# Optimization experiments

Measured on AMD Instinct MI355X. Metric: run time of the kernel, lower is better.

The kernel has to match this reference:

```python
import jax, jax.numpy as jnp
import numpy as np
from jax import lax

N_COMPONENTS = 50
K = 15
SIGMA = 1.0
N_ITERS = 100


def _pairwise_sq_dists(x):
    # squared euclidean distances, [N, N]
    sq = jnp.sum(x * x, axis=1)
    d2 = sq[:, None] + sq[None, :] - 2.0 * (x @ x.T)
    return jnp.maximum(d2, 0.0)


def _knn_affinity(d2, scale):
    # top-K smallest distances per row -> dense sparse-pattern affinity, row-normalized
    n = d2.shape[0]
    neg_topk, knn_idx = lax.top_k(-d2, K)          # [N, K]
    w = jnp.exp(-(-neg_topk) * scale)              # exp(-d^2 * scale) on kNN entries
    rows = jnp.arange(n)[:, None]
    mat = jnp.zeros_like(d2).at[rows, knn_idx].set(w)
    return mat / jnp.sum(mat, axis=1, keepdims=True)


def setup_inputs() -> dict:
    key = jax.random.key(0)
    expression = jax.random.normal(key, (4096, 1000), dtype=jnp.float32)
    return {"expression": expression}


def reference(expression):
    x = expression
    n = x.shape[0]

    # --- PCA via eigh of gene-gene covariance ---
    xc = x - jnp.mean(x, axis=0)
    cov = (xc.T @ xc) / (n - 1)                    # [G, G]
    evals, evecs = jnp.linalg.eigh(cov)            # ascending
    order = jnp.argsort(evals)[::-1]
    evecs = evecs[:, order]
    pca = xc @ evecs[:, :N_COMPONENTS]             # [N, C]

    d2 = _pairwise_sq_dists(pca)                   # [N, N]

    # transition matrix: exp(-d^2 / (2 sigma^2)) on kNN
    transition = _knn_affinity(d2, 1.0 / (2.0 * SIGMA ** 2))
    # pseudotime diffusion matrix: exp(-d^2) on kNN
    diff_mat = _knn_affinity(d2, 1.0)

    # power iteration from root cell 0
    d0 = jnp.zeros((n,), dtype=pca.dtype).at[0].set(1.0)

    def step(d, _):
        dn = diff_mat @ d
        dn = dn / jnp.max(dn)
        return dn, None

    pseudotime, _ = lax.scan(step, d0, None, length=N_ITERS)

    return (pseudotime.astype(jnp.float32),
            transition.astype(jnp.float32),
            pca.astype(jnp.float32))
```

## Files before the change

### kernel.cpp

```cpp
#include <hip/hip_runtime.h>
#include <math.h>
#include <stdint.h>

static const int NS = 4096;
static const int MF = 1000;
static const int NCOMP = 50;

#define TR_OFF  ((size_t)4096)
#define PCA_OFF ((size_t)4096 + (size_t)4096*4096)

__global__ void k_colsum(const float* __restrict__ x, float* __restrict__ part){
  int b = blockIdx.x, tid = threadIdx.x;
  float a0=0,a1=0,a2=0,a3=0;
  for (int r=b*64; r<b*64+64; r++){
    const float* row = x + (size_t)r*MF;
    if (tid      < MF) a0 += row[tid];
    if (tid+256  < MF) a1 += row[tid+256];
    if (tid+512  < MF) a2 += row[tid+512];
    if (tid+768  < MF) a3 += row[tid+768];
  }
  if (tid      < MF) part[b*MF+tid]     = a0;
  if (tid+256  < MF) part[b*MF+tid+256] = a1;
  if (tid+512  < MF) part[b*MF+tid+512] = a2;
  if (tid+768  < MF) part[b*MF+tid+768] = a3;
}

__global__ void k_colmean(const float* __restrict__ part, float* __restrict__ mean){
  int c = blockIdx.x*256 + threadIdx.x;
  if (c < MF){ float s=0; for (int b=0;b<64;b++) s += part[b*MF+c]; mean[c] = s/4096.0f; }
}

__global__ void k_cov(const float* __restrict__ x, const float* __restrict__ mean,
                      double* __restrict__ Ah){
  __shared__ float As[32][65];
  __shared__ float Bs[32][65];
  int i0 = blockIdx.y*64, j0 = blockIdx.x*64;
  int tx = threadIdx.x, ty = threadIdx.y;
  int tid = ty*16+tx;
  double acc[4][4];
  #pragma unroll
  for (int u=0;u<4;u++)
    #pragma unroll
    for (int v=0;v<4;v++) acc[u][v]=0.0;
  for (int k0=0;k0<4096;k0+=32){
    for (int t=tid;t<32*64;t+=256){
      int kk=t>>6, ii=t&63;
      int gi=i0+ii, gj=j0+ii;
      As[kk][ii] = (gi<MF) ? (x[(size_t)(k0+kk)*MF+gi]-mean[gi]) : 0.f;
      Bs[kk][ii] = (gj<MF) ? (x[(size_t)(k0+kk)*MF+gj]-mean[gj]) : 0.f;
    }
    __syncthreads();
    for (int kk=0;kk<32;kk++){
      float a[4], b[4];
      #pragma unroll
      for (int u=0;u<4;u++){ a[u]=As[kk][ty*4+u]; b[u]=Bs[kk][tx*4+u]; }
      #pragma unroll
      for (int u=0;u<4;u++)
        #pragma unroll
        for (int v=0;v<4;v++) acc[u][v] += (double)a[u]*(double)b[v];
    }
    __syncthreads();
  }
  #pragma unroll
  for (int u=0;u<4;u++)
    #pragma unroll
    for (int v=0;v<4;v++){
      int gi=i0+ty*4+u, gj=j0+tx*4+v;
      if (gi<MF && gj<MF) Ah[(size_t)gi*MF+gj] = acc[u][v]*(1.0/4095.0);
    }
}

__device__ __forceinline__ unsigned wang(unsigned s){
  s=(s^61u)^(s>>16); s*=9u; s^=s>>4; s*=0x27d4eb2du; s^=s>>15; return s;
}

__global__ void __launch_bounds__(256) k_hh_step(double* __restrict__ Ah,
                                                 double* __restrict__ Vh,
                                                 double* __restrict__ tauv,
                                                 double* __restrict__ betaH,
                                                 const double* __restrict__ w1prev,
                                                 double* __restrict__ w1next,
                                                 const double* __restrict__ colprev,
                                                 double* __restrict__ colnext,
                                                 int k){
  __shared__ double vprev[1000], wfull[1000], vk[1000];
  __shared__ double red4[4], redb[4];
  int tid = threadIdx.x;
  int lane = tid & 63, wv = tid >> 6;

  double vd = 0.0;
  if (k > 0){
    for (int j = k + tid; j < 1000; j += 256){
      double vv = Vh[(size_t)(k-1)*MF + j];
      double ww = w1prev[j];
      vprev[j] = vv;
      wfull[j] = ww;
      vd += vv*ww;
    }
  }
  #pragma unroll
  for (int off=32; off; off>>=1) vd += __shfl_down(vd, off, 64);
  if (lane==0) red4[wv] = vd;
  __syncthreads();
  double vdot = red4[0]+red4[1]+red4[2]+red4[3];
  double tp  = (k>0) ? tauv[k-1] : 0.0;
  double hts = 0.5*tp*tp*vdot;
  if (k > 0){
    for (int j = k + tid; j < 1000; j += 256)
      wfull[j] = tp*wfull[j] - hts*vprev[j];
  }
  __syncthreads();

  double a2 = 0.0;
  for (int j = k+1 + tid; j < 1000; j += 256){
    double c;
    if (k > 0) c = colprev[j] - (vprev[j]*wfull[k] + wfull[j]*vprev[k]);
    else       c = Ah[(size_t)j*MF + k];
    vk[j] = c;
    if (j > k+1) a2 += c*c;
  }
  #pragma unroll
  for (int off=32; off; off>>=1) a2 += __shfl_down(a2, off, 64);
  if (lane==0) redb[wv] = a2;
  __syncthreads();
  double xn2 = redb[0]+redb[1]+redb[2]+redb[3];
  double alpha = vk[k+1];
  double beta, tau, scl;
  if (xn2 == 0.0){ beta = alpha; tau = 0.0; scl = 0.0; }
  else {
    double nrm = sqrt(alpha*alpha + xn2);
    beta = (alpha >= 0.0) ? -nrm : nrm;
    tau  = (beta - alpha)/beta;
    scl  = 1.0/(alpha - beta);
  }
  if (tid==0 && blockIdx.x==0){
    tauv[k]=tau; betaH[k]=beta;
    if (k>0) Ah[(size_t)k*MF + k] -= 2.0*wfull[k];
  }
  for (int j = k+1 + tid; j < 1000; j += 256)
    vk[j] = (j == k+1) ? 1.0 : vk[j]*scl;
  __syncthreads();
  if (blockIdx.x==0){
    for (int j = k+1 + tid; j < 1000; j += 256)
      Vh[(size_t)k*MF + j] = vk[j];
  }

  int step = gridDim.x*4;
  for (int r = k+1 + blockIdx.x*4 + wv; r < 1000; r += step){
    double vr = (k>0)? vprev[r] : 0.0;
    double wr = (k>0)? wfull[r] : 0.0;
    double* row = Ah + (size_t)r*MF;
    double acc = 0.0;
    for (int c = k+1 + lane; c < 1000; c += 64){
      double a = row[c];
      if (k > 0){
        a -= vr*wfull[c] + wr*vprev[c];
        row[c] = a;
      }
      acc += a*vk[c];
      if (c == k+1) colnext[r] = a;
    }
    #pragma unroll
    for (int off=32; off; off>>=1) acc += __shfl_down(acc, off, 64);
    if (lane==0) w1next[r] = acc;
  }
}

__global__ void k_hh_fin(double* __restrict__ Ah, const double* __restrict__ Vh,
                         const double* __restrict__ tauv,
                         const double* __restrict__ w1last){
  if (threadIdx.x==0 && blockIdx.x==0){
    double v8 = Vh[(size_t)997*MF + 998];
    double v9 = Vh[(size_t)997*MF + 999];
    double w18 = w1last[998], w19 = w1last[999];
    double tau = tauv[997];
    double vdot = v8*w18 + v9*w19;
    double hts = 0.5*tau*tau*vdot;
    double w8 = tau*w18 - hts*v8;
    double w9 = tau*w19 - hts*v9;
    Ah[(size_t)998*MF+998] -= v8*w8 + w8*v8;
    Ah[(size_t)999*MF+998] -= v9*w8 + w9*v8;
    Ah[(size_t)999*MF+999] -= v9*w9 + w9*v9;
  }
}

__global__ void k_hh_extract(const double* __restrict__ Ah, double* __restrict__ alphaH,
                             double* __restrict__ betaH){
  int t = blockIdx.x*256 + threadIdx.x;
  if (t < MF) alphaH[t] = Ah[(size_t)t*MF+t];
  if (t == 0) betaH[998] = Ah[(size_t)999*MF+998];
}

__device__ __forceinline__ int sgnchg(double a, double b){
  return (int)(((unsigned long long)(__double_as_longlong(a) ^ __double_as_longlong(b))) >> 63);
}

__global__ void k_bisect(const double* __restrict__ alphaT, const double* __restrict__ betaT,
                         double* __restrict__ lamT){
  __shared__ double al[1000], ab[1000], bb[1000];
  int tid = threadIdx.x;
  for (int t=tid; t<1000; t+=64){
    double a = alphaT[t];
    double b = (t<999)? betaT[t] : 0.0;
    al[t]=a; ab[t]=fabs(b); bb[t]=b*b;
  }
  __syncthreads();
  if (tid >= NCOMP) return;
  int i = tid;
  double lo=1e300, hi=-1e300;
  for (int k2=0;k2<1000;k2++){
    double bl = (k2>0)? ab[k2-1] : 0.0;
    double br = (k2<999)? ab[k2] : 0.0;
    double a = al[k2];
    lo = fmin(lo, a-bl-br);
    hi = fmax(hi, a+bl+br);
  }
  int target = 999 - i;
  for (int it=0; it<55; it++){
    double mid = 0.5*(lo+hi);
    int cnt = 0;
    double d1 = 1.0;
    double d0 = al[0]-mid;
    cnt += (int)(((unsigned long long)__double_as_longlong(d0))>>63);
    int k2 = 1;
    for (; k2+3 < 1000; k2 += 4){
      double n0 = (al[k2  ]-mid)*d0 - bb[k2-1]*d1;
      double n1 = (al[k2+1]-mid)*n0 - bb[k2  ]*d0;
      double n2 = (al[k2+2]-mid)*n1 - bb[k2+1]*n0;
      double n3 = (al[k2+3]-mid)*n2 - bb[k2+2]*n1;
      cnt += sgnchg(n0,d0)+sgnchg(n1,n0)+sgnchg(n2,n1)+sgnchg(n3,n2);
      double mm = fmax(fabs(n3), fabs(n2));
      double s = (mm > 1e250) ? 1e-250 : ((mm < 1e-250) ? 1e250 : 1.0);
      d1 = n2*s; d0 = n3*s;
    }
    for (; k2 < 1000; k2++){
      double nn = (al[k2]-mid)*d0 - bb[k2-1]*d1;
      cnt += sgnchg(nn, d0);
      d1 = d0; d0 = nn;
    }
    if (cnt > target) hi = mid; else lo = mid;
  }
  lamT[i] = 0.5*(lo+hi);
}

__device__ void gtsv_serial(int m, double* dl, double* dd, double* du, double* x){
  for (int r=0;r<m-1;r++){
    if (fabs(dd[r]) >= fabs(dl[r])){
      if (dd[r] != 0.0){
        double fact = dl[r]/dd[r];
        dd[r+1] -= fact*du[r];
        x[r+1]  -= fact*x[r];
      }
      if (r < m-2) dl[r] = 0.0;
    } else {
      double fact = dd[r]/dl[r];
      dd[r] = dl[r];
      double tdd = dd[r+1];
      dd[r+1] = du[r] - fact*tdd;
      if (r < m-2){
        double tdu = du[r+1];
        dl[r] = tdu;
        du[r+1] = -fact*tdu;
      }
      du[r] = tdd;
      double t2 = x[r]; x[r] = x[r+1]; x[r+1] = t2 - fact*x[r+1];
    }
  }
  x[m-1] /= dd[m-1];
  if (m >= 2) x[m-2] = (x[m-2] - du[m-2]*x[m-1])/dd[m-2];
  for (int r=m-3;r>=0;r--)
    x[r] = (x[r] - du[r]*x[r+1] - dl[r]*x[r+2])/dd[r];
}

__global__ void __launch_bounds__(256) k_inviter(const double* __restrict__ alphaH,
                                                 const double* __restrict__ betaH,
                                                 const double* __restrict__ lamT,
                                                 double* __restrict__ V50,
                                                 double* __restrict__ lamR){
  __shared__ double v[1000], xx[1000], dd[1000], du[1000], dl[1000];
  __shared__ double red[256];
  int i = blockIdx.x, tid = threadIdx.x;
  double lam = lamT[i];
  for (int t=tid;t<1000;t+=256){
    unsigned h = wang((unsigned)(i*1000+t)*2654435761u + 777u);
    v[t] = (double)(h & 0xffffffu)/8388608.0 - 1.0;
  }
  __syncthreads();
  for (int it=0; it<3; it++){
    for (int t=tid;t<1000;t+=256){
      dd[t] = alphaH[t]-lam;
      if (t<999){ du[t]=betaH[t]; dl[t]=betaH[t]; }
      xx[t] = v[t];
    }
    __syncthreads();
    if (tid==0) gtsv_serial(1000, dl, dd, du, xx);
    __syncthreads();
    double a=0; for (int t=tid;t<1000;t+=256) a += xx[t]*xx[t];
    red[tid]=a; __syncthreads();
    for (int off=128;off;off>>=1){ if(tid<off) red[tid]+=red[tid+off]; __syncthreads(); }
    double inv = 1.0/sqrt(red[0]);
    __syncthreads();
    for (int t=tid;t<1000;t+=256) v[t]=xx[t]*inv;
    __syncthreads();
  }
  double a=0;
  for (int t=tid;t<1000;t+=256){
    double s = alphaH[t]*v[t];
    if (t>0)   s += betaH[t-1]*v[t-1];
    if (t<999) s += betaH[t]*v[t+1];
    a += v[t]*s;
  }
  red[tid]=a; __syncthreads();
  for (int off=128;off;off>>=1){ if(tid<off) red[tid]+=red[tid+off]; __syncthreads(); }
  if (tid==0) lamR[i]=red[0];
  for (int t=tid;t<1000;t+=256) V50[(size_t)i*1000+t]=v[t];
}

__global__ void __launch_bounds__(256) k_sign(const double* __restrict__ alphaH,
                                              const double* __restrict__ betaH,
                                              const double* __restrict__ V50,
                                              const double* __restrict__ lamR,
                                              float* __restrict__ sgnv){
  __shared__ double v[1000], xx[1000], dd[1000], du[1000], dl[1000];
  __shared__ double red[256];
  __shared__ double lam_s;
  __shared__ int ab[2];
  __shared__ float sig;
  int i = blockIdx.x, tid = threadIdx.x;
  for (int t=tid;t<1000;t+=256) v[t]=V50[(size_t)i*1000+t];
  if (tid==0){ lam_s=lamR[i]; ab[0]=0; ab[1]=1000; sig=1.f; }
  __syncthreads();
  while (true){
    int a=ab[0], b=ab[1];
    if (b-a <= 25) break;
    int c = a + (b-a)/2;
    double m1=0,m2=0;
    for (int t=a+tid;t<b;t+=256){ double q=v[t]*v[t]; if (t<c) m1+=q; else m2+=q; }
    red[tid]=m1; __syncthreads();
    for (int off=128;off;off>>=1){ if(tid<off) red[tid]+=red[tid+off]; __syncthreads(); }
    double M1=red[0]; __syncthreads();
    red[tid]=m2; __syncthreads();
    for (int off=128;off;off>>=1){ if(tid<off) red[tid]+=red[tid+off]; __syncthreads(); }
    double M2=red[0]; __syncthreads();
    double tot=M1+M2;
    if (fmin(M1,M2) <= 1e-10*tot){
      if (tid==0){ if (M1>=M2) ab[1]=c; else ab[0]=c; }
      __syncthreads();
      a=ab[0]; b=ab[1];
      double nn=0; for (int t=a+tid;t<b;t+=256) nn+=v[t]*v[t];
      red[tid]=nn; __syncthreads();
      for (int off=128;off;off>>=1){ if(tid<off) red[tid]+=red[tid+off]; __syncthreads(); }
      double inv = 1.0/sqrt(red[0]); __syncthreads();
      for (int t=a+tid;t<b;t+=256) v[t]*=inv;
      __syncthreads();
      for (int it=0; it<2; it++){
        for (int t=a+tid;t<b;t+=256){
          int L=t-a;
          dd[L]=alphaH[t]-lam_s;
          if (t<b-1){ du[L]=betaH[t]; dl[L]=betaH[t]; }
          xx[L]=v[t];
        }
        __syncthreads();
        if (tid==0) gtsv_serial(b-a, dl, dd, du, xx);
        __syncthreads();
        double s2=0; for (int t=a+tid;t<b;t+=256){ double q=xx[t-a]; s2+=q*q; }
        red[tid]=s2; __syncthreads();
        for (int off=128;off;off>>=1){ if(tid<off) red[tid]+=red[tid+off]; __syncthreads(); }
        double inv2 = 1.0/sqrt(red[0]); __syncthreads();
        for (int t=a+tid;t<b;t+=256) v[t]=xx[t-a]*inv2;
        __syncthreads();
      }
      double rq=0;
      for (int t=a+tid;t<b;t+=256){
        double s = alphaH[t]*v[t];
        if (t>a)   s += betaH[t-1]*v[t-1];
        if (t<b-1) s += betaH[t]*v[t+1];
        rq += v[t]*s;
      }
      red[tid]=rq; __syncthreads();
      for (int off=128;off;off>>=1){ if(tid<off) red[tid]+=red[tid+off]; __syncthreads(); }
      if (tid==0) lam_s=red[0];
      __syncthreads();
      continue;
    }
    if (tid==0){
      double vc1 = v[c-1], vc = v[c];
      if (fabs(vc1) >= fabs(vc)){
        sig = (vc1 < 0.0) ? 1.f : -1.f;
      } else {
        double req = (betaH[c-1] >= 0.0) ? -1.0 : 1.0;
        double have = (vc >= 0.0) ? 1.0 : -1.0;
        sig = (have == req) ? 1.f : -1.f;
      }
    }
    break;
  }
  __syncthreads();
  if (tid==0) sgnv[i]=sig;
}

__global__ void __launch_bounds__(256) k_applyQm(const double* __restrict__ Vh,
                                                 const double* __restrict__ tauv,
                                                 const double* __restrict__ V50,
                                                 const float* __restrict__ sgnv,
                                                 float* __restrict__ E50){
  __shared__ double u[1000];
  __shared__ double red4[4];
  int i = blockIdx.x, tid = threadIdx.x;
  int lane = tid & 63, wv = tid >> 6;
  for (int t=tid;t<1000;t+=256) u[t] = V50[(size_t)i*1000+t];
  __syncthreads();
  for (int k=997;k>=0;k--){
    const double* v = Vh + (size_t)k*MF;
    double vr[4];
    double a=0;
    #pragma unroll
    for (int s=0;s<4;s++){
      int j = k+1+tid+s*256;
      double vv = 0.0;
      if (j < 1000){ vv = v[j]; a += vv*u[j]; }
      vr[s] = vv;
    }
    #pragma unroll
    for (int off=32; off; off>>=1) a += __shfl_down(a, off, 64);
    if (lane==0) red4[wv] = a;
    __syncthreads();
    double td = tauv[k]*(red4[0]+red4[1]+red4[2]+red4[3]);
    #pragma unroll
    for (int s=0;s<4;s++){
      int j = k+1+tid+s*256;
      if (j < 1000) u[j] -= td*vr[s];
    }
    __syncthreads();
  }
  double s = (double)sgnv[i];
  for (int t=tid;t<1000;t+=256) E50[(size_t)t*NCOMP + i] = (float)(u[t]*s);
}

__global__ void k_pca(const float* __restrict__ x, const float* __restrict__ mean,
                      const float* __restrict__ E, float* __restrict__ P){
  __shared__ float As[64][65];
  __shared__ float Es[64][65];
  int r0 = blockIdx.x*64;
  int tx = threadIdx.x & 15, ty = threadIdx.x >> 4;
  float acc[4][4];
  #pragma unroll
  for (int u=0;u<4;u++)
    #pragma unroll
    for (int v=0;v<4;v++) acc[u][v]=0.f;
  for (int k0=0;k0<MF;k0+=64){
    for (int t=threadIdx.x;t<64*64;t+=256){
      int i=t>>6, kk=t&63; int k=k0+kk;
      As[i][kk] = (k<MF) ? (x[(size_t)(r0+i)*MF+k]-mean[k]) : 0.f;
    }
    for (int t=threadIdx.x;t<64*65;t+=256){
      int kk=t/65, c=t%65; int k=k0+kk;
      Es[kk][c] = (k<MF && c<NCOMP) ? E[(size_t)k*NCOMP+c] : 0.f;
    }
    __syncthreads();
    for (int kk=0;kk<64;kk++){
      float a[4], b[4];
      #pragma unroll
      for (int u=0;u<4;u++){ a[u]=As[ty*4+u][kk]; b[u]=Es[kk][tx*4+u]; }
      #pragma unroll
      for (int u=0;u<4;u++)
        #pragma unroll
        for (int v=0;v<4;v++) acc[u][v] += a[u]*b[v];
    }
    __syncthreads();
  }
  #pragma unroll
  for (int u=0;u<4;u++){
    int r=r0+ty*4+u;
    #pragma unroll
    for (int v=0;v<4;v++){
      int c=tx*4+v;
      if (c<NCOMP) P[(size_t)r*NCOMP+c] = acc[u][v];
    }
  }
}

__global__ void k_rowsq(const float* __restrict__ P, float* __restrict__ sqv){
  int r = blockIdx.x*256 + threadIdx.x;
  if (r < NS){
    float s=0;
    for (int c=0;c<NCOMP;c++){ float v=P[(size_t)r*NCOMP+c]; s+=v*v; }
    sqv[r]=s;
  }
}

__global__ void k_knn(const float* __restrict__ P, const float* __restrict__ sqv,
                      float* __restrict__ trans, int* __restrict__ kidx,
                      float* __restrict__ kwd){
  __shared__ float pi[64];
  __shared__ unsigned long long keys[16*256];
  __shared__ unsigned long long redk[4];
  __shared__ unsigned long long wink[15];
  __shared__ float wt[15], wd[15], sums[2];
  int i = blockIdx.x, tid = threadIdx.x;
  int lane = tid & 63, wv = tid >> 6;
  for (int t=tid;t<NCOMP;t+=256) pi[t] = P[(size_t)i*NCOMP+t];
  __syncthreads();
  float sqi = sqv[i];
  for (int s2=0;s2<16;s2++){
    int j = tid + s2*256;
    float dot=0;
    for (int c=0;c<NCOMP;c++) dot += pi[c]*P[(size_t)j*NCOMP+c];
    float d2 = sqi + sqv[j] - 2.f*dot;
    d2 = fmaxf(d2, 0.f);
    unsigned int db = __float_as_uint(d2);
    keys[s2*256+tid] = ((unsigned long long)db<<32) | (unsigned)j;
  }
  __syncthreads();
  for (int rsel=0;rsel<15;rsel++){
    unsigned long long m = ~0ull;
    #pragma unroll
    for (int s2=0;s2<16;s2++){
      unsigned long long k = keys[s2*256+tid];
      m = (k<m)?k:m;
    }
    #pragma unroll
    for (int off=32; off; off>>=1){
      unsigned long long o = __shfl_down(m, off, 64);
      m = (o<m)?o:m;
    }
    if (lane==0) redk[wv]=m;
    __syncthreads();
    unsigned long long w = redk[0];
    if (redk[1]<w) w=redk[1];
    if (redk[2]<w) w=redk[2];
    if (redk[3]<w) w=redk[3];
    if (tid==0) wink[rsel]=w;
    #pragma unroll
    for (int s2=0;s2<16;s2++)
      if (keys[s2*256+tid]==w) keys[s2*256+tid]=~0ull;
    __syncthreads();
  }
  if (tid<15){
    unsigned long long w = wink[tid];
    float d2 = __uint_as_float((unsigned)(w>>32));
    wt[tid] = expf(-0.5f*d2);
    wd[tid] = expf(-d2);
  }
  __syncthreads();
  if (tid==0){
    float st=0, sd=0;
    for (int k=0;k<15;k++){ st+=wt[k]; sd+=wd[k]; }
    sums[0]=st; sums[1]=sd;
  }
  __syncthreads();
  float* row = trans + (size_t)i*NS;
  for (int c=tid;c<NS;c+=256) row[c]=0.f;
  __syncthreads();
  if (tid<15){
    int j = (int)(wink[tid] & 0xffffffffull);
    row[j] = wt[tid]/sums[0];
    kidx[i*15+tid] = j;
    kwd[i*15+tid]  = wd[tid]/sums[1];
  }
}

__global__ void __launch_bounds__(1024) k_power(const int* __restrict__ kidx,
                                                const float* __restrict__ kwd,
                                                float* __restrict__ outPT){
  __shared__ float d[4096];
  __shared__ float dn[4096];
  __shared__ float red[16];
  int tid = threadIdx.x;
  int lane = tid & 63, wv = tid >> 6;
  for (int t=tid;t<4096;t+=1024) d[t] = (t==0)?1.f:0.f;
  __syncthreads();
  for (int it=0; it<100; it++){
    float lmax = 0.f;
    for (int r=tid;r<4096;r+=1024){
      float a=0;
      #pragma unroll
      for (int k=0;k<15;k++) a += kwd[r*15+k]*d[kidx[r*15+k]];
      dn[r]=a;
      lmax = fmaxf(lmax, a);
    }
    #pragma unroll
    for (int off=32; off; off>>=1) lmax = fmaxf(lmax, __shfl_down(lmax, off, 64));
    if (lane==0) red[wv]=lmax;
    __syncthreads();
    float m = red[0];
    #pragma unroll
    for (int w=1;w<16;w++) m = fmaxf(m, red[w]);
    for (int r=tid;r<4096;r+=1024) d[r]=dn[r]/m;
    __syncthreads();
  }
  for (int t=tid;t<4096;t+=1024) outPT[t]=d[t];
}

extern "C" void kernel_launch(void* const* d_in, const int* in_sizes, int n_in,
                              void* d_out, int out_size, void* d_ws, size_t ws_size,
                              hipStream_t stream){
  const float* x = (const float*)d_in[0];
  float* out = (float*)d_out;
  char* base = (char*)d_ws;

  double* Ah     = (double*)(base + 0);
  float*  sqv    = (float*) (base + 0);
  int*    kidx   = (int*)   (base + 16384);
  float*  kwd    = (float*) (base + 262144);
  double* Vh     = (double*)(base + 8000000);
  double* V50    = (double*)(base + 16000000);
  float*  E50    = (float*) (base + 16400000);
  float*  part   = (float*) (base + 16600000);
  float*  mean   = (float*) (base + 16856000);
  double* tauv   = (double*)(base + 16860000);
  double* betaH  = (double*)(base + 16868000);
  double* alphaH = (double*)(base + 16876000);
  double* w1a    = (double*)(base + 16884000);
  double* w1b    = (double*)(base + 16892000);
  double* cola   = (double*)(base + 16900000);
  double* colb   = (double*)(base + 16908000);
  double* lamT   = (double*)(base + 16916000);
  double* lamR   = (double*)(base + 16916400);
  float*  sgnv   = (float*) (base + 16916800);

  double* w1buf[2]  = { w1a, w1b };
  double* colbuf[2] = { cola, colb };

  k_colsum<<<64,256,0,stream>>>(x, part);
  k_colmean<<<4,256,0,stream>>>(part, mean);
  k_cov<<<dim3(16,16),dim3(16,16),0,stream>>>(x, mean, Ah);

  for (int k=0;k<998;k++){
    int m = 999-k;
    int g = (m+3)>>2;
    if (g > 250) g = 250;
    k_hh_step<<<g,256,0,stream>>>(Ah, Vh, tauv, betaH,
        w1buf[(k+1)&1], w1buf[k&1], colbuf[(k+1)&1], colbuf[k&1], k);
  }
  k_hh_fin<<<1,64,0,stream>>>(Ah, Vh, tauv, w1buf[997&1]);
  k_hh_extract<<<4,256,0,stream>>>(Ah, alphaH, betaH);

  k_bisect<<<1,64,0,stream>>>(alphaH, betaH, lamT);
  k_inviter<<<50,256,0,stream>>>(alphaH, betaH, lamT, V50, lamR);

  k_sign<<<50,256,0,stream>>>(alphaH, betaH, V50, lamR, sgnv);

  k_applyQm<<<50,256,0,stream>>>(Vh, tauv, V50, sgnv, E50);
  k_pca<<<64,256,0,stream>>>(x, mean, E50, out + PCA_OFF);
  k_rowsq<<<16,256,0,stream>>>(out + PCA_OFF, sqv);
  k_knn<<<4096,256,0,stream>>>(out + PCA_OFF, sqv, out + TR_OFF, kidx, kwd);
  k_power<<<1,1024,0,stream>>>(kidx, kwd, out);
}
```

Baseline: 15.82 ms.

## Fuse Householder tridiagonalization into one persistent kernel with grid barrier

Replaces 998 separate Householder step launches with one persistent 250-block kernel that synchronizes through an atomic grid barrier, keeping the previous reflector in shared memory. It also computes only the lower-triangular covariance tiles and mirrors them. It merges the finalize, extract and bisection kernels, and merges inverse iteration with sign fixing. applyQm now keeps the vector in registers with one barrier per step. The aim is to remove per-launch overhead and redundant work. The risk is that the software grid barrier deadlocks if all 250 blocks are not co-resident, and the spinning and fences add cost at every step.

New measurement: 39.51 ms. 150% more time.

```diff
diff --git a/kernel.cpp b/kernel.cpp
--- a/kernel.cpp
+++ b/kernel.cpp
@@ -8,6 +8,7 @@
 
 #define TR_OFF  ((size_t)4096)
 #define PCA_OFF ((size_t)4096 + (size_t)4096*4096)
+#define HH_GRID 250
 
 __global__ void k_colsum(const float* __restrict__ x, float* __restrict__ part){
   int b = blockIdx.x, tid = threadIdx.x;
@@ -30,11 +31,15 @@
   if (c < MF){ float s=0; for (int b=0;b<64;b++) s += part[b*MF+c]; mean[c] = s/4096.0f; }
 }
 
+__global__ void k_barinit(unsigned* bar){ if (threadIdx.x < 2) bar[threadIdx.x] = 0u; }
+
 __global__ void k_cov(const float* __restrict__ x, const float* __restrict__ mean,
                       double* __restrict__ Ah){
   __shared__ float As[32][65];
   __shared__ float Bs[32][65];
-  int i0 = blockIdx.y*64, j0 = blockIdx.x*64;
+  int bx = blockIdx.x, by = blockIdx.y;
+  if (bx > by) return;
+  int i0 = by*64, j0 = bx*64;
   int tx = threadIdx.x, ty = threadIdx.y;
   int tid = ty*16+tx;
   double acc[4][4];
@@ -66,7 +71,11 @@
     #pragma unroll
     for (int v=0;v<4;v++){
       int gi=i0+ty*4+u, gj=j0+tx*4+v;
-      if (gi<MF && gj<MF) Ah[(size_t)gi*MF+gj] = acc[u][v]*(1.0/4095.0);
+      if (gi<MF && gj<MF){
+        double val = acc[u][v]*(1.0/4095.0);
+        Ah[(size_t)gi*MF+gj] = val;
+        Ah[(size_t)gj*MF+gi] = val;
+      }
     }
 }
 
@@ -74,102 +83,135 @@
   s=(s^61u)^(s>>16); s*=9u; s^=s>>4; s*=0x27d4eb2du; s^=s>>15; return s;
 }
 
-__global__ void __launch_bounds__(256) k_hh_step(double* __restrict__ Ah,
-                                                 double* __restrict__ Vh,
-                                                 double* __restrict__ tauv,
-                                                 double* __restrict__ betaH,
-                                                 const double* __restrict__ w1prev,
-                                                 double* __restrict__ w1next,
-                                                 const double* __restrict__ colprev,
-                                                 double* __restrict__ colnext,
-                                                 int k){
-  __shared__ double vprev[1000], wfull[1000], vk[1000];
+__device__ __forceinline__ void grid_sync(unsigned* bar){
+  __syncthreads();
+  if (threadIdx.x == 0){
+    __threadfence();
+    unsigned gen = __hip_atomic_load(&bar[1], __ATOMIC_RELAXED, __HIP_MEMORY_SCOPE_AGENT);
+    unsigned prev = __hip_atomic_fetch_add(&bar[0], 1u, __ATOMIC_ACQ_REL, __HIP_MEMORY_SCOPE_AGENT);
+    if (prev + 1u == (unsigned)HH_GRID){
+      __hip_atomic_store(&bar[0], 0u, __ATOMIC_RELAXED, __HIP_MEMORY_SCOPE_AGENT);
+      __hip_atomic_fetch_add(&bar[1], 1u, __ATOMIC_RELEASE, __HIP_MEMORY_SCOPE_AGENT);
+    } else {
+      while (__hip_atomic_load(&bar[1], __ATOMIC_RELAXED, __HIP_MEMORY_SCOPE_AGENT) == gen)
+        __builtin_amdgcn_s_sleep(1);
+    }
+    __threadfence();
+  }
+  __syncthreads();
+}
+
+__global__ void __launch_bounds__(256) k_hh_all(double* Ah,
+                                                double* __restrict__ Vh,
+                                                double* __restrict__ tauv,
+                                                double* __restrict__ betaH,
+                                                double* w1a, double* w1b,
+                                                double* cola, double* colb,
+                                                unsigned* bar){
+  __shared__ double vbuf[2][1000];
+  __shared__ double wfull[1000];
   __shared__ double red4[4], redb[4];
+  __shared__ double sAlpha;
   int tid = threadIdx.x;
   int lane = tid & 63, wv = tid >> 6;
-
-  double vd = 0.0;
-  if (k > 0){
-    for (int j = k + tid; j < 1000; j += 256){
-      double vv = Vh[(size_t)(k-1)*MF + j];
-      double ww = w1prev[j];
-      vprev[j] = vv;
-      wfull[j] = ww;
-      vd += vv*ww;
-    }
-  }
-  #pragma unroll
-  for (int off=32; off; off>>=1) vd += __shfl_down(vd, off, 64);
-  if (lane==0) red4[wv] = vd;
-  __syncthreads();
-  double vdot = red4[0]+red4[1]+red4[2]+red4[3];
-  double tp  = (k>0) ? tauv[k-1] : 0.0;
-  double hts = 0.5*tp*tp*vdot;
-  if (k > 0){
-    for (int j = k + tid; j < 1000; j += 256)
-      wfull[j] = tp*wfull[j] - hts*vprev[j];
-  }
-  __syncthreads();
-
-  double a2 = 0.0;
-  for (int j = k+1 + tid; j < 1000; j += 256){
-    double c;
-    if (k > 0) c = colprev[j] - (vprev[j]*wfull[k] + wfull[j]*vprev[k]);
-    else       c = Ah[(size_t)j*MF + k];
-    vk[j] = c;
-    if (j > k+1) a2 += c*c;
-  }
-  #pragma unroll
-  for (int off=32; off; off>>=1) a2 += __shfl_down(a2, off, 64);
-  if (lane==0) redb[wv] = a2;
-  __syncthreads();
-  double xn2 = redb[0]+redb[1]+redb[2]+redb[3];
-  double alpha = vk[k+1];
-  double beta, tau, scl;
-  if (xn2 == 0.0){ beta = alpha; tau = 0.0; scl = 0.0; }
-  else {
-    double nrm = sqrt(alpha*alpha + xn2);
-    beta = (alpha >= 0.0) ? -nrm : nrm;
-    tau  = (beta - alpha)/beta;
-    scl  = 1.0/(alpha - beta);
-  }
-  if (tid==0 && blockIdx.x==0){
-    tauv[k]=tau; betaH[k]=beta;
-    if (k>0) Ah[(size_t)k*MF + k] -= 2.0*wfull[k];
-  }
-  for (int j = k+1 + tid; j < 1000; j += 256)
-    vk[j] = (j == k+1) ? 1.0 : vk[j]*scl;
-  __syncthreads();
-  if (blockIdx.x==0){
+  double tau_prev = 0.0;
+
+  for (int k = 0; k < 998; k++){
+    double* vk    = vbuf[k & 1];
+    double* vprev = vbuf[(k & 1) ^ 1];
+    const double* w1prev  = (k & 1) ? w1a : w1b;
+    double*       w1next  = (k & 1) ? w1b : w1a;
+    const double* colprev = (k & 1) ? cola : colb;
+    double*       colnext = (k & 1) ? colb : cola;
+
+    double vd = 0.0;
+    if (k > 0){
+      for (int j = k + tid; j < 1000; j += 256){
+        double ww = w1prev[j];
+        wfull[j] = ww;
+        vd += vprev[j]*ww;
+      }
+    }
+    #pragma unroll
+    for (int off=32; off; off>>=1) vd += __shfl_down(vd, off, 64);
+    if (lane==0) red4[wv] = vd;
+    __syncthreads();
+    double vdot = red4[0]+red4[1]+red4[2]+red4[3];
+    double tp  = tau_prev;
+    double hts = 0.5*tp*tp*vdot;
+    if (k > 0){
+      for (int j = k + tid; j < 1000; j += 256)
+        wfull[j] = tp*wfull[j] - hts*vprev[j];
+    }
+    __syncthreads();
+
+    double a2 = 0.0;
+    for (int j = k+1 + tid; j < 1000; j += 256){
+      double c;
+      if (k > 0) c = colprev[j] - (vprev[j]*wfull[k] + wfull[j]*vprev[k]);
+      else       c = Ah[(size_t)j*MF + k];
+      vk[j] = c;
+      if (j == k+1) sAlpha = c;
+      if (j > k+1) a2 += c*c;
+    }
+    #pragma unroll
+    for (int off=32; off; off>>=1) a2 += __shfl_down(a2, off, 64);
+    if (lane==0) redb[wv] = a2;
+    __syncthreads();
+    double xn2 = redb[0]+redb[1]+redb[2]+redb[3];
+    double alpha = sAlpha;
+    double beta, tau, scl;
+    if (xn2 == 0.0){ beta = alpha; tau = 0.0; scl = 0.0; }
+    else {
+      double nrm = sqrt(alpha*alpha + xn2);
+      beta = (alpha >= 0.0) ? -nrm : nrm;
+      tau  = (beta - alpha)/beta;
+      scl  = 1.0/(alpha - beta);
+    }
+    if (tid==0 && blockIdx.x==0){
+      tauv[k]=tau; betaH[k]=beta;
+      if (k>0) Ah[(size_t)k*MF + k] -= 2.0*wfull[k];
+    }
     for (int j = k+1 + tid; j < 1000; j += 256)
-      Vh[(size_t)k*MF + j] = vk[j];
-  }
-
-  int step = gridDim.x*4;
-  for (int r = k+1 + blockIdx.x*4 + wv; r < 1000; r += step){
-    double vr = (k>0)? vprev[r] : 0.0;
-    double wr = (k>0)? wfull[r] : 0.0;
-    double* row = Ah + (size_t)r*MF;
-    double acc = 0.0;
-    for (int c = k+1 + lane; c < 1000; c += 64){
-      double a = row[c];
-      if (k > 0){
-        a -= vr*wfull[c] + wr*vprev[c];
-        row[c] = a;
-      }
-      acc += a*vk[c];
-      if (c == k+1) colnext[r] = a;
-    }
-    #pragma unroll
-    for (int off=32; off; off>>=1) acc += __shfl_down(acc, off, 64);
-    if (lane==0) w1next[r] = acc;
-  }
-}
-
-__global__ void k_hh_fin(double* __restrict__ Ah, const double* __restrict__ Vh,
-                         const double* __restrict__ tauv,
-                         const double* __restrict__ w1last){
-  if (threadIdx.x==0 && blockIdx.x==0){
+      vk[j] = (j == k+1) ? 1.0 : vk[j]*scl;
+    __syncthreads();
+    if (blockIdx.x==0){
+      for (int j = k+1 + tid; j < 1000; j += 256)
+        Vh[(size_t)k*MF + j] = vk[j];
+    }
+
+    for (int r = k+1 + blockIdx.x*4 + wv; r < 1000; r += HH_GRID*4){
+      double vr = (k>0)? vprev[r] : 0.0;
+      double wr = (k>0)? wfull[r] : 0.0;
+      double* row = Ah + (size_t)r*MF;
+      double acc = 0.0;
+      for (int c = k+1 + lane; c < 1000; c += 64){
+        double a = row[c];
+        if (k > 0){ a -= vr*wfull[c] + wr*vprev[c]; row[c] = a; }
+        acc += a*vk[c];
+        if (c == k+1) colnext[r] = a;
+      }
+      #pragma unroll
+      for (int off=32; off; off>>=1) acc += __shfl_down(acc, off, 64);
+      if (lane==0) w1next[r] = acc;
+    }
+
+    grid_sync(bar);
+    tau_prev = tau;
+  }
+}
+
+__device__ __forceinline__ int sgnchg(double a, double b){
+  return (int)(((unsigned long long)(__double_as_longlong(a) ^ __double_as_longlong(b))) >> 63);
+}
+
+__global__ void k_post(double* __restrict__ Ah, const double* __restrict__ Vh,
+                       const double* __restrict__ tauv, const double* __restrict__ w1last,
+                       double* __restrict__ alphaH, double* __restrict__ betaH,
+                       double* __restrict__ lamT){
+  __shared__ double al[1000], abv[1000], bb[1000];
+  int tid = threadIdx.x;
+  if (tid==0){
     double v8 = Vh[(size_t)997*MF + 998];
     double v9 = Vh[(size_t)997*MF + 999];
     double w18 = w1last[998], w19 = w1last[999];
@@ -182,35 +224,24 @@
     Ah[(size_t)999*MF+998] -= v9*w8 + w9*v8;
     Ah[(size_t)999*MF+999] -= v9*w9 + w9*v9;
   }
-}
-
-__global__ void k_hh_extract(const double* __restrict__ Ah, double* __restrict__ alphaH,
-                             double* __restrict__ betaH){
-  int t = blockIdx.x*256 + threadIdx.x;
-  if (t < MF) alphaH[t] = Ah[(size_t)t*MF+t];
-  if (t == 0) betaH[998] = Ah[(size_t)999*MF+998];
-}
-
-__device__ __forceinline__ int sgnchg(double a, double b){
-  return (int)(((unsigned long long)(__double_as_longlong(a) ^ __double_as_longlong(b))) >> 63);
-}
-
-__global__ void k_bisect(const double* __restrict__ alphaT, const double* __restrict__ betaT,
-                         double* __restrict__ lamT){
-  __shared__ double al[1000], ab[1000], bb[1000];
-  int tid = threadIdx.x;
-  for (int t=tid; t<1000; t+=64){
-    double a = alphaT[t];
-    double b = (t<999)? betaT[t] : 0.0;
-    al[t]=a; ab[t]=fabs(b); bb[t]=b*b;
+  __syncthreads();
+  for (int t=tid;t<1000;t+=64){
+    double a2 = Ah[(size_t)t*MF+t];
+    alphaH[t]=a2; al[t]=a2;
+  }
+  if (tid==0) betaH[998] = Ah[(size_t)999*MF+998];
+  __syncthreads();
+  for (int t=tid;t<1000;t+=64){
+    double b = (t<999)? betaH[t] : 0.0;
+    abv[t]=fabs(b); bb[t]=b*b;
   }
   __syncthreads();
   if (tid >= NCOMP) return;
   int i = tid;
   double lo=1e300, hi=-1e300;
   for (int k2=0;k2<1000;k2++){
-    double bl = (k2>0)? ab[k2-1] : 0.0;
-    double br = (k2<999)? ab[k2] : 0.0;
+    double bl = (k2>0)? abv[k2-1] : 0.0;
+    double br = (k2<999)? abv[k2] : 0.0;
     double a = al[k2];
     lo = fmin(lo, a-bl-br);
     hi = fmax(hi, a+bl+br);
@@ -272,13 +303,16 @@
     x[r] = (x[r] - du[r]*x[r+1] - dl[r]*x[r+2])/dd[r];
 }
 
-__global__ void __launch_bounds__(256) k_inviter(const double* __restrict__ alphaH,
+__global__ void __launch_bounds__(256) k_invsign(const double* __restrict__ alphaH,
                                                  const double* __restrict__ betaH,
                                                  const double* __restrict__ lamT,
                                                  double* __restrict__ V50,
-                                                 double* __restrict__ lamR){
+                                                 float* __restrict__ sgnv){
   __shared__ double v[1000], xx[1000], dd[1000], du[1000], dl[1000];
   __shared__ double red[256];
+  __shared__ double lam_s;
+  __shared__ int ab[2];
+  __shared__ float sig;
   int i = blockIdx.x, tid = threadIdx.x;
   double lam = lamT[i];
   for (int t=tid;t<1000;t+=256){
@@ -312,30 +346,15 @@
   }
   red[tid]=a; __syncthreads();
   for (int off=128;off;off>>=1){ if(tid<off) red[tid]+=red[tid+off]; __syncthreads(); }
-  if (tid==0) lamR[i]=red[0];
+  if (tid==0){ lam_s = red[0]; ab[0]=0; ab[1]=1000; sig=1.f; }
   for (int t=tid;t<1000;t+=256) V50[(size_t)i*1000+t]=v[t];
-}
-
-__global__ void __launch_bounds__(256) k_sign(const double* __restrict__ alphaH,
-                                              const double* __restrict__ betaH,
-                                              const double* __restrict__ V50,
-                                              const double* __restrict__ lamR,
-                                              float* __restrict__ sgnv){
-  __shared__ double v[1000], xx[1000], dd[1000], du[1000], dl[1000];
-  __shared__ double red[256];
-  __shared__ double lam_s;
-  __shared__ int ab[2];
-  __shared__ float sig;
-  int i = blockIdx.x, tid = threadIdx.x;
-  for (int t=tid;t<1000;t+=256) v[t]=V50[(size_t)i*1000+t];
-  if (tid==0){ lam_s=lamR[i]; ab[0]=0; ab[1]=1000; sig=1.f; }
   __syncthreads();
   while (true){
-    int a=ab[0], b=ab[1];
-    if (b-a <= 25) break;
-    int c = a + (b-a)/2;
+    int a0=ab[0], b0=ab[1];
+    if (b0-a0 <= 25) break;
+    int c = a0 + (b0-a0)/2;
     double m1=0,m2=0;
-    for (int t=a+tid;t<b;t+=256){ double q=v[t]*v[t]; if (t<c) m1+=q; else m2+=q; }
+    for (int t=a0+tid;t<b0;t+=256){ double q=v[t]*v[t]; if (t<c) m1+=q; else m2+=q; }
     red[tid]=m1; __syncthreads();
     for (int off=128;off;off>>=1){ if(tid<off) red[tid]+=red[tid+off]; __syncthreads(); }
     double M1=red[0]; __syncthreads();
@@ -346,35 +365,35 @@
     if (fmin(M1,M2) <= 1e-10*tot){
       if (tid==0){ if (M1>=M2) ab[1]=c; else ab[0]=c; }
       __syncthreads();
-      a=ab[0]; b=ab[1];
-      double nn=0; for (int t=a+tid;t<b;t+=256) nn+=v[t]*v[t];
+      a0=ab[0]; b0=ab[1];
+      double nn=0; for (int t=a0+tid;t<b0;t+=256) nn+=v[t]*v[t];
       red[tid]=nn; __syncthreads();
       for (int off=128;off;off>>=1){ if(tid<off) red[tid]+=red[tid+off]; __syncthreads(); }
       double inv = 1.0/sqrt(red[0]); __syncthreads();
-      for (int t=a+tid;t<b;t+=256) v[t]*=inv;
+      for (int t=a0+tid;t<b0;t+=256) v[t]*=inv;
       __syncthreads();
       for (int it=0; it<2; it++){
-        for (int t=a+tid;t<b;t+=256){
-          int L=t-a;
+        for (int t=a0+tid;t<b0;t+=256){
+          int L=t-a0;
           dd[L]=alphaH[t]-lam_s;
-          if (t<b-1){ du[L]=betaH[t]; dl[L]=betaH[t]; }
+          if (t<b0-1){ du[L]=betaH[t]; dl[L]=betaH[t]; }
           xx[L]=v[t];
         }
         __syncthreads();
-        if (tid==0) gtsv_serial(b-a, dl, dd, du, xx);
+        if (tid==0) gtsv_serial(b0-a0, dl, dd, du, xx);
         __syncthreads();
-        double s2=0; for (int t=a+tid;t<b;t+=256){ double q=xx[t-a]; s2+=q*q; }
+        double s2=0; for (int t=a0+tid;t<b0;t+=256){ double q=xx[t-a0]; s2+=q*q; }
         red[tid]=s2; __syncthreads();
         for (int off=128;off;off>>=1){ if(tid<off) red[tid]+=red[tid+off]; __syncthreads(); }
         double inv2 = 1.0/sqrt(red[0]); __syncthreads();
-        for (int t=a+tid;t<b;t+=256) v[t]=xx[t-a]*inv2;
+        for (int t=a0+tid;t<b0;t+=256) v[t]=xx[t-a0]*inv2;
         __syncthreads();
       }
       double rq=0;
-      for (int t=a+tid;t<b;t+=256){
+      for (int t=a0+tid;t<b0;t+=256){
         double s = alphaH[t]*v[t];
-        if (t>a)   s += betaH[t-1]*v[t-1];
-        if (t<b-1) s += betaH[t]*v[t+1];
+        if (t>a0)   s += betaH[t-1]*v[t-1];
+        if (t<b0-1) s += betaH[t]*v[t+1];
         rq += v[t]*s;
       }
       red[tid]=rq; __syncthreads();
@@ -404,37 +423,41 @@
                                                  const double* __restrict__ V50,
                                                  const float* __restrict__ sgnv,
                                                  float* __restrict__ E50){
-  __shared__ double u[1000];
-  __shared__ double red4[4];
+  __shared__ double red2[2][4];
+  __shared__ double tl[1000];
   int i = blockIdx.x, tid = threadIdx.x;
   int lane = tid & 63, wv = tid >> 6;
-  for (int t=tid;t<1000;t+=256) u[t] = V50[(size_t)i*1000+t];
+  int base = tid*4;
+  for (int t=tid;t<1000;t+=256) tl[t] = tauv[t];
+  const double* src = V50 + (size_t)i*1000;
+  double u0=0,u1=0,u2=0,u3=0;
+  if (base < 1000){
+    u0 = src[base]; u1 = src[base+1]; u2 = src[base+2]; u3 = src[base+3];
+  }
   __syncthreads();
   for (int k=997;k>=0;k--){
     const double* v = Vh + (size_t)k*MF;
-    double vr[4];
-    double a=0;
-    #pragma unroll
-    for (int s=0;s<4;s++){
-      int j = k+1+tid+s*256;
-      double vv = 0.0;
-      if (j < 1000){ vv = v[j]; a += vv*u[j]; }
-      vr[s] = vv;
+    double a = 0.0, v0=0,v1=0,v2=0,v3=0;
+    if (base < 1000 && base+3 >= k+1){
+      if (base   >= k+1){ v0 = v[base  ]; a += v0*u0; }
+      if (base+1 >= k+1){ v1 = v[base+1]; a += v1*u1; }
+      if (base+2 >= k+1){ v2 = v[base+2]; a += v2*u2; }
+      if (base+3 >= k+1){ v3 = v[base+3]; a += v3*u3; }
     }
     #pragma unroll
     for (int off=32; off; off>>=1) a += __shfl_down(a, off, 64);
-    if (lane==0) red4[wv] = a;
-    __syncthreads();
-    double td = tauv[k]*(red4[0]+red4[1]+red4[2]+red4[3]);
-    #pragma unroll
-    for (int s=0;s<4;s++){
-      int j = k+1+tid+s*256;
-      if (j < 1000) u[j] -= td*vr[s];
-    }
-    __syncthreads();
+    if (lane==0) red2[k&1][wv] = a;
+    __syncthreads();
+    double td = tl[k]*(red2[k&1][0]+red2[k&1][1]+red2[k&1][2]+red2[k&1][3]);
+    u0 -= td*v0; u1 -= td*v1; u2 -= td*v2; u3 -= td*v3;
   }
   double s = (double)sgnv[i];
-  for (int t=tid;t<1000;t+=256) E50[(size_t)t*NCOMP + i] = (float)(u[t]*s);
+  if (base < 1000){
+    E50[(size_t)(base  )*NCOMP + i] = (float)(u0*s);
+    E50[(size_t)(base+1)*NCOMP + i] = (float)(u1*s);
+    E50[(size_t)(base+2)*NCOMP + i] = (float)(u2*s);
+    E50[(size_t)(base+3)*NCOMP + i] = (float)(u3*s);
+  }
 }
 
 __global__ void k_pca(const float* __restrict__ x, const float* __restrict__ mean,
@@ -616,30 +639,19 @@
   double* cola   = (double*)(base + 16900000);
   double* colb   = (double*)(base + 16908000);
   double* lamT   = (double*)(base + 16916000);
-  double* lamR   = (double*)(base + 16916400);
-  float*  sgnv   = (float*) (base + 16916800);
-
-  double* w1buf[2]  = { w1a, w1b };
-  double* colbuf[2] = { cola, colb };
+  float*  sgnv   = (float*) (base + 16916400);
+  unsigned* bar  = (unsigned*)(base + 16917000);
 
   k_colsum<<<64,256,0,stream>>>(x, part);
   k_colmean<<<4,256,0,stream>>>(part, mean);
+  k_barinit<<<1,64,0,stream>>>(bar);
   k_cov<<<dim3(16,16),dim3(16,16),0,stream>>>(x, mean, Ah);
 
-  for (int k=0;k<998;k++){
-    int m = 999-k;
-    int g = (m+3)>>2;
-    if (g > 250) g = 250;
-    k_hh_step<<<g,256,0,stream>>>(Ah, Vh, tauv, betaH,
-        w1buf[(k+1)&1], w1buf[k&1], colbuf[(k+1)&1], colbuf[k&1], k);
-  }
-  k_hh_fin<<<1,64,0,stream>>>(Ah, Vh, tauv, w1buf[997&1]);
-  k_hh_extract<<<4,256,0,stream>>>(Ah, alphaH, betaH);
-
-  k_bisect<<<1,64,0,stream>>>(alphaH, betaH, lamT);
-  k_inviter<<<50,256,0,stream>>>(alphaH, betaH, lamT, V50, lamR);
-
-  k_sign<<<50,256,0,stream>>>(alphaH, betaH, V50, lamR, sgnv);
+  k_hh_all<<<HH_GRID,256,0,stream>>>(Ah, Vh, tauv, betaH, w1a, w1b, cola, colb, bar);
+
+  k_post<<<1,64,0,stream>>>(Ah, Vh, tauv, w1b, alphaH, betaH, lamT);
+
+  k_invsign<<<50,256,0,stream>>>(alphaH, betaH, lamT, V50, sgnv);
 
   k_applyQm<<<50,256,0,stream>>>(Vh, tauv, V50, sgnv, E50);
   k_pca<<<64,256,0,stream>>>(x, mean, E50, out + PCA_OFF);
```
